# Kernel tuning notes

Measured on AMD Instinct MI355X. Metric: run time of the kernel, lower is better.

Reference implementation:

```python
import jax, jax.numpy as jnp
import numpy as np
import math

B, S, E, H = 4, 1024, 1024, 16
HD = E // H
MAX_SEQ = 5000
THETA = 10000.0


def _freqs_cis():
    # RotaryPositionalEncoding buffer: complex64 [MAX_SEQ, E//2]
    freqs = 1.0 / (THETA ** (np.arange(0, E, 2)[: E // 2] / E))
    ang = np.outer(np.arange(MAX_SEQ), freqs)
    return jnp.asarray(np.exp(1j * ang).astype(np.complex64))


def _rope(x, idx, fc_table):
    # x: [B, S, E]; pairs consecutive channels across the FULL embed_dim
    # (applied before head splitting, faithful to the original module)
    xc = x.reshape(*x.shape[:-1], -1, 2)
    xc = jax.lax.complex(xc[..., 0], xc[..., 1])  # [B, S, E//2]
    out = xc * fc_table[idx]                       # [B, S, E//2]
    return jnp.stack([jnp.real(out), jnp.imag(out)], axis=-1).reshape(x.shape)


def reference(query, key, value, query_index, key_index, attn_mask,
              key_padding_mask, Wq, bq, Wk, bk, Wv, bv, Wo, bo):
    q = query @ Wq.T + bq
    k = key @ Wk.T + bk
    v = value @ Wv.T + bv

    fc = _freqs_cis()
    q = _rope(q, query_index, fc)
    k = _rope(k, key_index, fc)

    # torch: q = cat(q.chunk(H, dim=-1), dim=0) -> flat HEAD-MAJOR [H*B, S, HD]
    qf = q.reshape(B, S, H, HD).transpose(2, 0, 1, 3).reshape(H * B, S, HD)
    kf = k.reshape(B, S, H, HD).transpose(2, 0, 1, 3).reshape(H * B, S, HD)
    vf = v.reshape(B, S, H, HD).transpose(2, 0, 1, 3).reshape(H * B, S, HD)

    # mask: logical_or(attn_mask[Sq,Sk], kpm[B,1,Sk]) -> [B, Sq, Sk]
    m = jnp.logical_or(attn_mask[None, :, :], key_padding_mask[:, None, :])
    madd = jnp.where(m, -jnp.inf, 0.0).astype(query.dtype)
    # torch repeat_interleave(H, dim=0) yields BATCH-MAJOR flat [B*H, Sq, Sk];
    # it is added to the head-major scores as-is (faithful to the original
    # indexing, including its head/batch-order quirk)
    madd_flat = jnp.repeat(madd, H, axis=0)

    scores = jnp.einsum('nqd,nkd->nqk', qf / math.sqrt(HD), kf) + madd_flat
    w = jax.nn.softmax(scores, axis=-1)              # [H*B, Sq, Sk]
    of = jnp.einsum('nqk,nkd->nqd', w, vf)           # [H*B, Sq, HD]

    # cat(chunks(dim=0), dim=-1) -> [B, Sq, E], head-major last dim
    attn_output = of.reshape(H, B, S, HD).transpose(1, 2, 0, 3).reshape(B, S, E)
    attn_output = attn_output @ Wo.T + bo

    # stack(chunks(dim=0), dim=1).mean(1) -> [B, Sq, Sk]
    attn_weights = w.reshape(H, B, S, S).transpose(1, 0, 2, 3).mean(axis=1)
    return attn_output, attn_weights


def setup_inputs() -> dict:
    key0 = jax.random.key(0)
    ks = jax.random.split(key0, 10)
    sc = 0.02
    inp = {
        'query': jax.random.normal(ks[0], (B, S, E), jnp.float32),
        'key': jax.random.normal(ks[1], (B, S, E), jnp.float32),
        'value': jax.random.normal(ks[2], (B, S, E), jnp.float32),
        'query_index': jnp.sort(jax.random.randint(ks[3], (B, S), 0, 4096), axis=-1),
        'key_index': jnp.sort(jax.random.randint(ks[4], (B, S), 0, 4096), axis=-1),
        'attn_mask': jnp.triu(jnp.ones((S, S), jnp.bool_), k=1),  # causal
        'key_padding_mask': jnp.zeros((B, S), jnp.bool_),
        'Wq': jax.random.normal(ks[5], (E, E), jnp.float32) * sc,
        'bq': jnp.zeros((E,), jnp.float32),
        'Wk': jax.random.normal(ks[6], (E, E), jnp.float32) * sc,
        'bk': jnp.zeros((E,), jnp.float32),
        'Wv': jax.random.normal(ks[7], (E, E), jnp.float32) * sc,
        'bv': jnp.zeros((E,), jnp.float32),
        'Wo': jax.random.normal(ks[8], (E, E), jnp.float32) * sc,
        'bo': jnp.zeros((E,), jnp.float32),
    }
    return inp
```

## Files before the change

kernel.cpp:

```cpp
#include <hip/hip_runtime.h>
#include <stdint.h>
#include <math.h>

#define B_ 4
#define S_ 1024
#define E_ 1024
#define H_ 16
#define HD_ 64
#define HB_ 64

typedef __attribute__((ext_vector_type(8))) short bhalf8;
typedef __attribute__((ext_vector_type(4))) float floatx4;

__device__ __forceinline__ unsigned short f2bf(float f) {
  union { float f; unsigned u; } v; v.f = f;
  unsigned r = (v.u + 0x7FFFu + ((v.u >> 16) & 1u)) >> 16;
  return (unsigned short)r;
}
__device__ __forceinline__ float bf2f(unsigned short b) {
  union { unsigned u; float f; } v; v.u = ((unsigned)b) << 16;
  return v.f;
}
__device__ __forceinline__ unsigned cvtpk_bf16(float a, float b) {
  unsigned r;
  asm volatile("v_cvt_pk_bf16_f32 %0, %1, %2" : "=v"(r) : "v"(a), "v"(b));
  return r;
}

__device__ __forceinline__ void gload16(const void* g, void* l) {
  __builtin_amdgcn_global_load_lds(
      (const __attribute__((address_space(1))) unsigned int*)g,
      (__attribute__((address_space(3))) unsigned int*)l, 16, 0, 0);
}

template <int NCH>
__device__ __forceinline__ void stage_tile(const unsigned short* org,
                                           unsigned short* lds, int wave, int lane) {
  const int rl = lane >> 3;
  const int scb = ((lane & 7) << 4) ^ (rl << 4);
  const char* base = (const char*)org + scb;
#pragma unroll
  for (int i = 0; i < NCH / 4; ++i) {
    const int c = wave + 4 * i;
    gload16(base + (size_t)(c * 8 + rl) * 2048, (char*)lds + c * 1024);
  }
}

__device__ __forceinline__ bhalf8 read_frag(const unsigned short* lds, int row, int kbyte) {
  const int off = row * 128 + (kbyte ^ ((row & 7) << 4));
  return *(const bhalf8*)((const char*)lds + off);
}

__global__ void detect_bool_kernel(const uint8_t* __restrict__ amask, int* __restrict__ flag) {
  if (threadIdx.x == 0 && blockIdx.x == 0) *flag = (amask[1] != 0) ? 1 : 0;
}

__global__ __launch_bounds__(256) void mprep_kernel(
    const void* __restrict__ amask, const void* __restrict__ kpm,
    const int* __restrict__ flagp, unsigned long long* __restrict__ Mbits) {
  const int gid = blockIdx.x * 256 + threadIdx.x;
  const int word = gid & 15, q = (gid >> 4) & 1023, bp = gid >> 14;
  const int k0 = word * 64;
  unsigned long long bits = 0;
  if (*flagp) {
    const uint8_t* ap = (const uint8_t*)amask + (size_t)q * 1024 + k0;
    const uint8_t* kp = (const uint8_t*)kpm + (size_t)bp * 1024 + k0;
#pragma unroll
    for (int c = 0; c < 4; ++c) {
      uint4 a = *(const uint4*)(ap + c * 16);
      uint4 k = *(const uint4*)(kp + c * 16);
      unsigned aw[4] = {a.x | k.x, a.y | k.y, a.z | k.z, a.w | k.w};
#pragma unroll
      for (int wv = 0; wv < 4; ++wv)
#pragma unroll
        for (int bt = 0; bt < 4; ++bt)
          if ((aw[wv] >> (8 * bt)) & 0xffu)
            bits |= 1ull << (c * 16 + wv * 4 + bt);
    }
  } else {
    const int* ap = (const int*)amask + (size_t)q * 1024 + k0;
    const int* kp = (const int*)kpm + (size_t)bp * 1024 + k0;
#pragma unroll
    for (int c = 0; c < 16; ++c) {
      int4 a = *(const int4*)(ap + c * 4);
      int4 k = *(const int4*)(kp + c * 4);
      if (a.x | k.x) bits |= 1ull << (c * 4 + 0);
      if (a.y | k.y) bits |= 1ull << (c * 4 + 1);
      if (a.z | k.z) bits |= 1ull << (c * 4 + 2);
      if (a.w | k.w) bits |= 1ull << (c * 4 + 3);
    }
  }
  Mbits[((size_t)bp << 14) + (size_t)q * 16 + word] = bits;
}

__global__ __launch_bounds__(256) void cvt_in_kernel(
    const float* __restrict__ q, const float* __restrict__ k,
    const float* __restrict__ v, unsigned short* __restrict__ Ab) {
  const int z = blockIdx.z;
  const float* src = (z == 0) ? q : (z == 1) ? k : v;
  unsigned short* dst = Ab + (size_t)z * 4194304;
  const size_t i = ((size_t)blockIdx.x * 256 + threadIdx.x) * 8;
  float4 a = *(const float4*)(src + i);
  float4 b = *(const float4*)(src + i + 4);
  bhalf8 r;
  r[0] = (short)f2bf(a.x); r[1] = (short)f2bf(a.y);
  r[2] = (short)f2bf(a.z); r[3] = (short)f2bf(a.w);
  r[4] = (short)f2bf(b.x); r[5] = (short)f2bf(b.y);
  r[6] = (short)f2bf(b.z); r[7] = (short)f2bf(b.w);
  *(bhalf8*)(dst + i) = r;
}

__global__ __launch_bounds__(256) void cvt_w_kernel(
    const float* __restrict__ wq, const float* __restrict__ wk,
    const float* __restrict__ wv, const float* __restrict__ wo,
    unsigned short* __restrict__ Wb) {
  const int z = blockIdx.z;
  const float* src = (z == 0) ? wq : (z == 1) ? wk : (z == 2) ? wv : wo;
  unsigned short* dst = Wb + (size_t)z * 1048576;
  const size_t i = ((size_t)blockIdx.x * 256 + threadIdx.x) * 8;
  float4 a = *(const float4*)(src + i);
  float4 b = *(const float4*)(src + i + 4);
  bhalf8 r;
  r[0] = (short)f2bf(a.x); r[1] = (short)f2bf(a.y);
  r[2] = (short)f2bf(a.z); r[3] = (short)f2bf(a.w);
  r[4] = (short)f2bf(b.x); r[5] = (short)f2bf(b.y);
  r[6] = (short)f2bf(b.z); r[7] = (short)f2bf(b.w);
  *(bhalf8*)(dst + i) = r;
}

template <bool BF16OUT>
__global__ __launch_bounds__(256) void mfma_gemm_kernel(
    const unsigned short* __restrict__ A0, const unsigned short* __restrict__ A1,
    const unsigned short* __restrict__ A2,
    const unsigned short* __restrict__ W0, const unsigned short* __restrict__ W1,
    const unsigned short* __restrict__ W2,
    const float* __restrict__ b0, const float* __restrict__ b1,
    const float* __restrict__ b2,
    void* __restrict__ C0, void* __restrict__ C1, void* __restrict__ C2) {
  const int z = blockIdx.z;
  const unsigned short* A = (z == 0) ? A0 : (z == 1) ? A1 : A2;
  const unsigned short* W = (z == 0) ? W0 : (z == 1) ? W1 : W2;
  const float* bias = (z == 0) ? b0 : (z == 1) ? b1 : b2;
  void* C = (z == 0) ? C0 : (z == 1) ? C1 : C2;
  const int lin = blockIdx.y * 8 + blockIdx.x;
  const int swz = (lin & 7) * 32 + (lin >> 3);
  const int m0 = (swz >> 3) * 128, n0 = (swz & 7) * 128;
  __shared__ unsigned short As[128 * 64];
  __shared__ unsigned short Ws[128 * 64];
  const int t = threadIdx.x, wave = t >> 6, lane = t & 63;
  const int wr = wave >> 1, wc = wave & 1;
  floatx4 acc[4][4];
  const floatx4 z4 = {0.f, 0.f, 0.f, 0.f};
#pragma unroll
  for (int i = 0; i < 4; ++i)
#pragma unroll
    for (int j = 0; j < 4; ++j) acc[i][j] = z4;

  for (int k0 = 0; k0 < 1024; k0 += 64) {
    stage_tile<16>(A + (size_t)m0 * 1024 + k0, As, wave, lane);
    stage_tile<16>(W + (size_t)n0 * 1024 + k0, Ws, wave, lane);
    __syncthreads();
#pragma unroll
    for (int ks = 0; ks < 2; ++ks) {
      const int kb = ks * 64 + ((lane >> 4) << 4);
      bhalf8 af[4], bf[4];
#pragma unroll
      for (int mi = 0; mi < 4; ++mi)
        af[mi] = read_frag(As, wr * 64 + mi * 16 + (lane & 15), kb);
#pragma unroll
      for (int ni = 0; ni < 4; ++ni)
        bf[ni] = read_frag(Ws, wc * 64 + ni * 16 + (lane & 15), kb);
#pragma unroll
      for (int mi = 0; mi < 4; ++mi)
#pragma unroll
        for (int ni = 0; ni < 4; ++ni)
          acc[mi][ni] = __builtin_amdgcn_mfma_f32_16x16x32_bf16(af[mi], bf[ni], acc[mi][ni], 0, 0, 0);
    }
    __syncthreads();
  }
#pragma unroll
  for (int mi = 0; mi < 4; ++mi)
#pragma unroll
    for (int ni = 0; ni < 4; ++ni) {
      const int col = n0 + wc * 64 + ni * 16 + (lane & 15);
      const float bv = bias[col];
#pragma unroll
      for (int r = 0; r < 4; ++r) {
        const int row = m0 + wr * 64 + mi * 16 + (lane >> 4) * 4 + r;
        const float v = acc[mi][ni][r] + bv;
        if (BF16OUT)
          ((unsigned short*)C)[(size_t)row * 1024 + col] = f2bf(v);
        else
          ((float*)C)[(size_t)row * 1024 + col] = v;
      }
    }
}

__global__ __launch_bounds__(256) void rope_bf_kernel(unsigned int* __restrict__ X,
                                                      const int* __restrict__ idxs) {
  const int gid = blockIdx.x * 256 + threadIdx.x;
  const int i = gid & 511, bs = gid >> 9;
  const int pos = idxs[bs];
  const double freq = exp(-(double)(2 * i) * (9.210340371976184 / 1024.0));
  const double ang = fmod((double)pos * freq, 6.283185307179586476925287);
  const float fa = (float)ang;
  float sn, c;
  sincosf(fa, &sn, &c);
  const unsigned v = X[gid];
  const float x = bf2f((unsigned short)(v & 0xffffu));
  const float y = bf2f((unsigned short)(v >> 16));
  const float rx = x * c - y * sn;
  const float ry = x * sn + y * c;
  X[gid] = (unsigned)f2bf(rx) | ((unsigned)f2bf(ry) << 16);
}

__global__ __launch_bounds__(256) void transpose_v_kernel(
    const unsigned short* __restrict__ Vr, unsigned short* __restrict__ Vt) {
  const int s0 = blockIdx.x * 64;
  const int bh = blockIdx.y;
  const int b = bh >> 4, h = bh & 15;
  __shared__ unsigned short L[64][72];
  const int t = threadIdx.x, r = t >> 2, cq = (t & 3) * 16;
  const unsigned short* src = Vr + ((size_t)(b * S_) + s0 + r) * E_ + h * HD_ + cq;
  *(bhalf8*)&L[r][cq] = *(const bhalf8*)src;
  *(bhalf8*)&L[r][cq + 8] = *(const bhalf8*)(src + 8);
  __syncthreads();
  bhalf8 o0, o1;
#pragma unroll
  for (int u = 0; u < 8; ++u) o0[u] = (short)L[cq + u][r];
#pragma unroll
  for (int u = 0; u < 8; ++u) o1[u] = (short)L[cq + 8 + u][r];
  unsigned short* dst = Vt + ((size_t)bh * 64 + r) * 1024 + s0 + cq;
  *(bhalf8*)dst = o0;
  *(bhalf8*)(dst + 8) = o1;
}

__global__ __launch_bounds__(256) void scores_sm_kernel(
    const unsigned short* __restrict__ Qr, const unsigned short* __restrict__ Kr,
    unsigned short* __restrict__ P, const unsigned long long* __restrict__ Mbits,
    int hb0, int nwg) {
  const int lin = blockIdx.y * 64 + blockIdx.x;
  const int q8 = nwg >> 3;
  const int swz = (lin & 7) * q8 + (lin >> 3);
  const int qb = swz & 63, lhb = swz >> 6;
  const int hb = hb0 + lhb;
  const int h = hb >> 2, b = hb & 3, bp = hb >> 4;
  const int q0 = qb * 16;
  __shared__ unsigned short Sbuf[16 * 1024];
  float* rptr = (float*)Sbuf;
  const int t = threadIdx.x, w = t >> 6, lane = t & 63;
  const int l4 = lane >> 4, l15 = lane & 15;

  const char* Qb = (const char*)Qr + ((size_t)b << 21) + h * 128;
  const char* Kb = (const char*)Kr + ((size_t)b << 21) + h * 128;

  const unsigned long long* mrow =
      Mbits + ((size_t)bp << 14) + (size_t)(q0 + l15) * 16 + w * 4;
  unsigned long long mw0 = mrow[0], mw1 = mrow[1], mw2 = mrow[2], mw3 = mrow[3];

  bhalf8 bq0 = *(const bhalf8*)(Qb + (size_t)(q0 + l15) * 2048 + l4 * 16);
  bhalf8 bq1 = *(const bhalf8*)(Qb + (size_t)(q0 + l15) * 2048 + 64 + l4 * 16);

  floatx4 acc[16];
  const floatx4 z4 = {0.f, 0.f, 0.f, 0.f};
#pragma unroll
  for (int i = 0; i < 16; ++i) acc[i] = z4;
#pragma unroll
  for (int mt = 0; mt < 16; ++mt) {
    const char* kr = Kb + (size_t)(w * 256 + mt * 16 + l15) * 2048 + l4 * 16;
    bhalf8 a0 = *(const bhalf8*)kr;
    bhalf8 a1 = *(const bhalf8*)(kr + 64);
    acc[mt] = __builtin_amdgcn_mfma_f32_16x16x32_bf16(a0, bq0, acc[mt], 0, 0, 0);
    acc[mt] = __builtin_amdgcn_mfma_f32_16x16x32_bf16(a1, bq1, acc[mt], 0, 0, 0);
  }

  float red[16];
#pragma unroll
  for (int mt = 0; mt < 16; ++mt)
    red[mt] = fmaxf(fmaxf(acc[mt][0], acc[mt][1]), fmaxf(acc[mt][2], acc[mt][3]));
#pragma unroll
  for (int s2 = 8; s2 > 0; s2 >>= 1)
#pragma unroll
    for (int i = 0; i < 8; ++i)
      if (i < s2) red[i] = fmaxf(red[i], red[i + s2]);
  float mx = red[0];
  mx = fmaxf(mx, __shfl_xor(mx, 16));
  mx = fmaxf(mx, __shfl_xor(mx, 32));
  if (l4 == 0) rptr[w * 16 + l15] = mx;
  __syncthreads();
  mx = fmaxf(fmaxf(rptr[l15], rptr[16 + l15]), fmaxf(rptr[32 + l15], rptr[48 + l15]));

  const float Cc = 0.18033688011112042f;
  const float mc = mx * Cc;
#pragma unroll
  for (int mt = 0; mt < 16; ++mt) {
    const unsigned long long mwv = (mt < 4) ? mw0 : (mt < 8) ? mw1 : (mt < 12) ? mw2 : mw3;
    const unsigned bits = (unsigned)(mwv >> ((mt & 3) * 16 + l4 * 4)) & 0xFu;
#pragma unroll
    for (int r = 0; r < 4; ++r) {
      float e = exp2f(__builtin_fmaf(acc[mt][r], Cc, -mc));
      acc[mt][r] = ((bits >> r) & 1u) ? 0.f : e;
    }
  }

#pragma unroll
  for (int mt = 0; mt < 16; ++mt)
    red[mt] = (acc[mt][0] + acc[mt][1]) + (acc[mt][2] + acc[mt][3]);
#pragma unroll
  for (int s2 = 8; s2 > 0; s2 >>= 1)
#pragma unroll
    for (int i = 0; i < 8; ++i)
      if (i < s2) red[i] += red[i + s2];
  float sm = red[0];
  sm += __shfl_xor(sm, 16);
  sm += __shfl_xor(sm, 32);
  if (l4 == 0) rptr[64 + w * 16 + l15] = sm;
  __syncthreads();
  sm = (rptr[64 + l15] + rptr[80 + l15]) + (rptr[96 + l15] + rptr[112 + l15]);
  const float inv = 1.0f / sm;
  __syncthreads();

  const int xr = (l15 & 7) << 4;
#pragma unroll
  for (int mt = 0; mt < 16; ++mt) {
    uint2 pk;
    pk.x = cvtpk_bf16(acc[mt][0] * inv, acc[mt][1] * inv);
    pk.y = cvtpk_bf16(acc[mt][2] * inv, acc[mt][3] * inv);
    const int kb2 = (w * 256 + mt * 16 + l4 * 4) * 2;
    *(uint2*)((char*)Sbuf + l15 * 2048 + (kb2 ^ xr)) = pk;
  }
  __syncthreads();

  unsigned short* pbase = P + ((size_t)lhb << 20);
#pragma unroll
  for (int rr = 0; rr < 4; ++rr) {
    const int ql = w * 4 + rr;
    const int gq = q0 + ql;
    const int xq = (ql & 7) << 4;
#pragma unroll
    for (int j = 0; j < 2; ++j) {
      bhalf8 v = *(const bhalf8*)((const char*)Sbuf + ql * 2048 +
                                  ((j * 1024 + lane * 16) ^ xq));
      *(bhalf8*)(pbase + ((size_t)gq << 10) + j * 512 + lane * 8) = v;
    }
  }
}

__global__ __launch_bounds__(256) void wmean_kernel(
    const unsigned short* __restrict__ P, float* __restrict__ outW,
    int nhh, int first) {
  const size_t gid = (size_t)blockIdx.x * 256 + threadIdx.x;
  const int k8 = (int)(gid & 127);
  const int q = (int)((gid >> 7) & 1023);
  const int b = (int)(gid >> 17);
  float s[8];
#pragma unroll
  for (int u = 0; u < 8; ++u) s[u] = 0.f;
  for (int hh = 0; hh < nhh; ++hh) {
    const int lhb = hh * 4 + b;
    bhalf8 v = *(const bhalf8*)(P + ((size_t)lhb << 20) + ((size_t)q << 10) + k8 * 8);
#pragma unroll
    for (int u = 0; u < 8; ++u) s[u] += bf2f((unsigned short)v[u]);
  }
  float* o = outW + (((size_t)(b * S_ + q)) << 10) + k8 * 8;
  const float invH = 1.0f / 16.0f;
  float4 v0, v1;
  v0.x = s[0] * invH; v0.y = s[1] * invH; v0.z = s[2] * invH; v0.w = s[3] * invH;
  v1.x = s[4] * invH; v1.y = s[5] * invH; v1.z = s[6] * invH; v1.w = s[7] * invH;
  if (!first) {
    float4 a = *(float4*)o, b4 = *(float4*)(o + 4);
    v0.x += a.x; v0.y += a.y; v0.z += a.z; v0.w += a.w;
    v1.x += b4.x; v1.y += b4.y; v1.z += b4.z; v1.w += b4.w;
  }
  *(float4*)o = v0;
  *(float4*)(o + 4) = v1;
}

__global__ __launch_bounds__(256) void pv_mfma_kernel(
    const unsigned short* __restrict__ Wt, const unsigned short* __restrict__ Vt,
    unsigned short* __restrict__ Ocat, int hb0, int nwg) {
  const int lin = blockIdx.y * 16 + blockIdx.x;
  const int q8 = nwg >> 3;
  const int swz = (lin & 7) * q8 + (lin >> 3);
  const int qt = swz & 15, lhb = swz >> 4;
  const int hb = hb0 + lhb;
  const int h = hb >> 2, b = hb & 3;
  const int q0 = qt * 64;
  __shared__ unsigned short Ps[64 * 64];
  __shared__ unsigned short Vs[64 * 64];
  const int t = threadIdx.x, wave = t >> 6, lane = t & 63;
  const int wr = wave >> 1, wc = wave & 1;
  const unsigned short* Wh = Wt + ((size_t)lhb << 20);
  const unsigned short* Vh = Vt + (size_t)(b * 16 + h) * 65536;
  floatx4 acc[2][2];
  const floatx4 z4 = {0.f, 0.f, 0.f, 0.f};
#pragma unroll
  for (int i = 0; i < 2; ++i)
#pragma unroll
    for (int j = 0; j < 2; ++j) acc[i][j] = z4;

  for (int k0 = 0; k0 < 1024; k0 += 64) {
    stage_tile<8>(Wh + (size_t)q0 * 1024 + k0, Ps, wave, lane);
    stage_tile<8>(Vh + k0, Vs, wave, lane);
    __syncthreads();
#pragma unroll
    for (int ks = 0; ks < 2; ++ks) {
      const int kb = ks * 64 + ((lane >> 4) << 4);
      bhalf8 af[2], bf[2];
#pragma unroll
      for (int mi = 0; mi < 2; ++mi)
        af[mi] = read_frag(Ps, wr * 32 + mi * 16 + (lane & 15), kb);
#pragma unroll
      for (int ni = 0; ni < 2; ++ni)
        bf[ni] = read_frag(Vs, wc * 32 + ni * 16 + (lane & 15), kb);
#pragma unroll
      for (int mi = 0; mi < 2; ++mi)
#pragma unroll
        for (int ni = 0; ni < 2; ++ni)
          acc[mi][ni] = __builtin_amdgcn_mfma_f32_16x16x32_bf16(af[mi], bf[ni], acc[mi][ni], 0, 0, 0);
    }
    __syncthreads();
  }
#pragma unroll
  for (int mi = 0; mi < 2; ++mi)
#pragma unroll
    for (int ni = 0; ni < 2; ++ni) {
      const int d = wc * 32 + ni * 16 + (lane & 15);
#pragma unroll
      for (int r = 0; r < 4; ++r) {
        const int q = q0 + wr * 32 + mi * 16 + (lane >> 4) * 4 + r;
        Ocat[((size_t)(b * S_) + q) * E_ + h * HD_ + d] = f2bf(acc[mi][ni][r]);
      }
    }
}

extern "C" void kernel_launch(void* const* d_in, const int* in_sizes, int n_in,
                              void* d_out, int out_size, void* d_ws, size_t ws_size,
                              hipStream_t stream) {
  (void)in_sizes; (void)n_in; (void)out_size;
  const float* query = (const float*)d_in[0];
  const float* key   = (const float*)d_in[1];
  const float* value = (const float*)d_in[2];
  const int* qidx = (const int*)d_in[3];
  const int* kidx = (const int*)d_in[4];
  const void* amask = d_in[5];
  const void* kpm   = d_in[6];
  const float* Wq = (const float*)d_in[7];
  const float* bq = (const float*)d_in[8];
  const float* Wk = (const float*)d_in[9];
  const float* bk = (const float*)d_in[10];
  const float* Wv = (const float*)d_in[11];
  const float* bv = (const float*)d_in[12];
  const float* Wo = (const float*)d_in[13];
  const float* bo = (const float*)d_in[14];

  float* outA = (float*)d_out;
  float* outW = (float*)d_out + (size_t)B_ * S_ * E_;

  float* ws = (float*)d_ws;
  unsigned short* Ab   = (unsigned short*)(ws + 0);
  unsigned short* Wb   = (unsigned short*)(ws + 6291456);
  unsigned short* Qr   = (unsigned short*)(ws + 8388608);
  unsigned short* Kr   = (unsigned short*)(ws + 10485760);
  unsigned short* Vr   = (unsigned short*)(ws + 12582912);
  unsigned short* Vt   = (unsigned short*)(ws + 14680064);
  unsigned short* Ocat = (unsigned short*)(ws + 16777216);
  int* flagp           = (int*)(ws + 18874368);
  unsigned long long* Mbits = (unsigned long long*)(ws + 18874432);
  const size_t tail_off = 18874432 + 131072;

  const size_t ws_floats = ws_size / 4;
  int CH = 0;
  unsigned short* P = nullptr;
  for (int c = 64; c >= 8; c >>= 1) {
    if (tail_off + (size_t)c * 524288 <= ws_floats) {
      CH = c;
      P = (unsigned short*)(ws + tail_off);
      break;
    }
  }
  if (!CH) {
    CH = 8;
    P = (unsigned short*)ws;
  }

  detect_bool_kernel<<<1, 64, 0, stream>>>((const uint8_t*)amask, flagp);
  mprep_kernel<<<256, 256, 0, stream>>>(amask, kpm, flagp, Mbits);

  cvt_in_kernel<<<dim3(2048, 1, 3), 256, 0, stream>>>(query, key, value, Ab);
  cvt_w_kernel<<<dim3(512, 1, 4), 256, 0, stream>>>(Wq, Wk, Wv, Wo, Wb);

  mfma_gemm_kernel<true><<<dim3(8, 32, 3), 256, 0, stream>>>(
      Ab, Ab + 4194304, Ab + 8388608,
      Wb, Wb + 1048576, Wb + 2097152,
      bq, bk, bv, Qr, Kr, Vr);

  rope_bf_kernel<<<8192, 256, 0, stream>>>((unsigned int*)Qr, qidx);
  rope_bf_kernel<<<8192, 256, 0, stream>>>((unsigned int*)Kr, kidx);

  transpose_v_kernel<<<dim3(16, 64), 256, 0, stream>>>(Vr, Vt);

  const int nch = HB_ / CH;
  for (int c = 0; c < nch; ++c) {
    const int hb0 = c * CH;
    scores_sm_kernel<<<dim3(64, CH), 256, 0, stream>>>(Qr, Kr, P, Mbits, hb0,
                                                       64 * CH);
    wmean_kernel<<<2048, 256, 0, stream>>>(P, outW, CH / 4, (c == 0) ? 1 : 0);
    pv_mfma_kernel<<<dim3(16, CH), 256, 0, stream>>>(P, Vt, Ocat, hb0, 16 * CH);
  }

  mfma_gemm_kernel<false><<<dim3(8, 32, 1), 256, 0, stream>>>(
      Ocat, Ocat, Ocat, Wb + 3145728, Wb + 3145728, Wb + 3145728,
      bo, bo, bo, outA, outA, outA);
}
```

Measured before the change: 241.3 us.

## Fuse conversion launches, write V transposed from GEMM, merge RoPE in float

Merges the input and weight bf16 conversion kernels into one launch and the two RoPE launches into one. The QKV GEMM epilogue now stores V directly in the per-head transposed layout, removing the separate transpose kernel. The GEMM block swizzle is extended across the z dimension, and the RoPE angle is computed in single precision with exp2f instead of double exp/fmod. This cuts launches, memory passes and FP64 work, at the cost of lower angle precision for large positions and strided stores in the V epilogue.

```diff
diff --git a/kernel.cpp b/kernel.cpp
--- a/kernel.cpp
+++ b/kernel.cpp
@@ -93,12 +93,24 @@
   Mbits[((size_t)bp << 14) + (size_t)q * 16 + word] = bits;
 }
 
-__global__ __launch_bounds__(256) void cvt_in_kernel(
+__global__ __launch_bounds__(256) void cvt_all_kernel(
     const float* __restrict__ q, const float* __restrict__ k,
-    const float* __restrict__ v, unsigned short* __restrict__ Ab) {
+    const float* __restrict__ v,
+    const float* __restrict__ wq, const float* __restrict__ wk,
+    const float* __restrict__ wv, const float* __restrict__ wo,
+    unsigned short* __restrict__ Ab, unsigned short* __restrict__ Wb) {
   const int z = blockIdx.z;
-  const float* src = (z == 0) ? q : (z == 1) ? k : v;
-  unsigned short* dst = Ab + (size_t)z * 4194304;
+  if (z >= 3 && blockIdx.x >= 512) return;
+  const float* src;
+  unsigned short* dst;
+  if (z < 3) {
+    src = (z == 0) ? q : (z == 1) ? k : v;
+    dst = Ab + (size_t)z * 4194304;
+  } else {
+    const int zz = z - 3;
+    src = (zz == 0) ? wq : (zz == 1) ? wk : (zz == 2) ? wv : wo;
+    dst = Wb + (size_t)zz * 1048576;
+  }
   const size_t i = ((size_t)blockIdx.x * 256 + threadIdx.x) * 8;
   float4 a = *(const float4*)(src + i);
   float4 b = *(const float4*)(src + i + 4);
@@ -110,25 +122,7 @@
   *(bhalf8*)(dst + i) = r;
 }
 
-__global__ __launch_bounds__(256) void cvt_w_kernel(
-    const float* __restrict__ wq, const float* __restrict__ wk,
-    const float* __restrict__ wv, const float* __restrict__ wo,
-    unsigned short* __restrict__ Wb) {
-  const int z = blockIdx.z;
-  const float* src = (z == 0) ? wq : (z == 1) ? wk : (z == 2) ? wv : wo;
-  unsigned short* dst = Wb + (size_t)z * 1048576;
-  const size_t i = ((size_t)blockIdx.x * 256 + threadIdx.x) * 8;
-  float4 a = *(const float4*)(src + i);
-  float4 b = *(const float4*)(src + i + 4);
-  bhalf8 r;
-  r[0] = (short)f2bf(a.x); r[1] = (short)f2bf(a.y);
-  r[2] = (short)f2bf(a.z); r[3] = (short)f2bf(a.w);
-  r[4] = (short)f2bf(b.x); r[5] = (short)f2bf(b.y);
-  r[6] = (short)f2bf(b.z); r[7] = (short)f2bf(b.w);
-  *(bhalf8*)(dst + i) = r;
-}
-
-template <bool BF16OUT>
+template <bool QKV>
 __global__ __launch_bounds__(256) void mfma_gemm_kernel(
     const unsigned short* __restrict__ A0, const unsigned short* __restrict__ A1,
     const unsigned short* __restrict__ A2,
@@ -137,18 +131,22 @@
     const float* __restrict__ b0, const float* __restrict__ b1,
     const float* __restrict__ b2,
     void* __restrict__ C0, void* __restrict__ C1, void* __restrict__ C2) {
-  const int z = blockIdx.z;
-  const unsigned short* A = (z == 0) ? A0 : (z == 1) ? A1 : A2;
-  const unsigned short* W = (z == 0) ? W0 : (z == 1) ? W1 : W2;
-  const float* bias = (z == 0) ? b0 : (z == 1) ? b1 : b2;
-  void* C = (z == 0) ? C0 : (z == 1) ? C1 : C2;
-  const int lin = blockIdx.y * 8 + blockIdx.x;
-  const int swz = (lin & 7) * 32 + (lin >> 3);
-  const int m0 = (swz >> 3) * 128, n0 = (swz & 7) * 128;
+  const int nb = gridDim.z * 256;
+  const int chunk = nb >> 3;
+  const int g = blockIdx.z * 256 + blockIdx.y * 8 + blockIdx.x;
+  const int swz = (g & 7) * chunk + (g >> 3);
+  const int zt = swz >> 8;
+  const int r8 = swz & 255;
+  const int m0 = (r8 >> 3) * 128, n0 = (r8 & 7) * 128;
+  const unsigned short* A = (zt == 0) ? A0 : (zt == 1) ? A1 : A2;
+  const unsigned short* W = (zt == 0) ? W0 : (zt == 1) ? W1 : W2;
+  const float* bias = (zt == 0) ? b0 : (zt == 1) ? b1 : b2;
+  void* C = (zt == 0) ? C0 : (zt == 1) ? C1 : C2;
   __shared__ unsigned short As[128 * 64];
   __shared__ unsigned short Ws[128 * 64];
   const int t = threadIdx.x, wave = t >> 6, lane = t & 63;
   const int wr = wave >> 1, wc = wave & 1;
+  const int l4 = lane >> 4, l15 = lane & 15;
   floatx4 acc[4][4];
   const floatx4 z4 = {0.f, 0.f, 0.f, 0.f};
 #pragma unroll
@@ -162,14 +160,14 @@
     __syncthreads();
 #pragma unroll
     for (int ks = 0; ks < 2; ++ks) {
-      const int kb = ks * 64 + ((lane >> 4) << 4);
+      const int kb = ks * 64 + (l4 << 4);
       bhalf8 af[4], bf[4];
 #pragma unroll
       for (int mi = 0; mi < 4; ++mi)
-        af[mi] = read_frag(As, wr * 64 + mi * 16 + (lane & 15), kb);
+        af[mi] = read_frag(As, wr * 64 + mi * 16 + l15, kb);
 #pragma unroll
       for (int ni = 0; ni < 4; ++ni)
-        bf[ni] = read_frag(Ws, wc * 64 + ni * 16 + (lane & 15), kb);
+        bf[ni] = read_frag(Ws, wc * 64 + ni * 16 + l15, kb);
 #pragma unroll
       for (int mi = 0; mi < 4; ++mi)
 #pragma unroll
@@ -178,61 +176,65 @@
     }
     __syncthreads();
   }
-#pragma unroll
-  for (int mi = 0; mi < 4; ++mi)
-#pragma unroll
-    for (int ni = 0; ni < 4; ++ni) {
-      const int col = n0 + wc * 64 + ni * 16 + (lane & 15);
-      const float bv = bias[col];
-#pragma unroll
-      for (int r = 0; r < 4; ++r) {
-        const int row = m0 + wr * 64 + mi * 16 + (lane >> 4) * 4 + r;
-        const float v = acc[mi][ni][r] + bv;
-        if (BF16OUT)
-          ((unsigned short*)C)[(size_t)row * 1024 + col] = f2bf(v);
-        else
-          ((float*)C)[(size_t)row * 1024 + col] = v;
+
+  if (QKV && zt == 2) {
+#pragma unroll
+    for (int mi = 0; mi < 4; ++mi) {
+      const int row0 = m0 + wr * 64 + mi * 16 + l4 * 4;
+      const int b = row0 >> 10, s = row0 & 1023;
+#pragma unroll
+      for (int ni = 0; ni < 4; ++ni) {
+        const int col = n0 + wc * 64 + ni * 16 + l15;
+        const int h = col >> 6, d = col & 63;
+        const float bv = bias[col];
+        ushort4 o;
+        o.x = f2bf(acc[mi][ni][0] + bv);
+        o.y = f2bf(acc[mi][ni][1] + bv);
+        o.z = f2bf(acc[mi][ni][2] + bv);
+        o.w = f2bf(acc[mi][ni][3] + bv);
+        *(ushort4*)((unsigned short*)C +
+                    (((size_t)(b * 16 + h) * 64 + d) << 10) + s) = o;
       }
     }
-}
-
-__global__ __launch_bounds__(256) void rope_bf_kernel(unsigned int* __restrict__ X,
-                                                      const int* __restrict__ idxs) {
+  } else {
+#pragma unroll
+    for (int mi = 0; mi < 4; ++mi)
+#pragma unroll
+      for (int ni = 0; ni < 4; ++ni) {
+        const int col = n0 + wc * 64 + ni * 16 + l15;
+        const float bv = bias[col];
+#pragma unroll
+        for (int r = 0; r < 4; ++r) {
+          const int row = m0 + wr * 64 + mi * 16 + l4 * 4 + r;
+          const float v = acc[mi][ni][r] + bv;
+          if (QKV)
+            ((unsigned short*)C)[(size_t)row * 1024 + col] = f2bf(v);
+          else
+            ((float*)C)[(size_t)row * 1024 + col] = v;
+        }
+      }
+  }
+}
+
+__global__ __launch_bounds__(256) void rope_bf_kernel(
+    unsigned int* __restrict__ Q, unsigned int* __restrict__ K,
+    const int* __restrict__ qidx, const int* __restrict__ kidx) {
+  const int z = blockIdx.y;
+  unsigned int* X = z ? K : Q;
+  const int* idxs = z ? kidx : qidx;
   const int gid = blockIdx.x * 256 + threadIdx.x;
   const int i = gid & 511, bs = gid >> 9;
   const int pos = idxs[bs];
-  const double freq = exp(-(double)(2 * i) * (9.210340371976184 / 1024.0));
-  const double ang = fmod((double)pos * freq, 6.283185307179586476925287);
-  const float fa = (float)ang;
+  const float fr = exp2f((float)i * (-13.287712379549449f / 512.0f));
+  const float ang = (float)pos * fr;
   float sn, c;
-  sincosf(fa, &sn, &c);
+  sincosf(ang, &sn, &c);
   const unsigned v = X[gid];
   const float x = bf2f((unsigned short)(v & 0xffffu));
   const float y = bf2f((unsigned short)(v >> 16));
   const float rx = x * c - y * sn;
   const float ry = x * sn + y * c;
   X[gid] = (unsigned)f2bf(rx) | ((unsigned)f2bf(ry) << 16);
-}
-
-__global__ __launch_bounds__(256) void transpose_v_kernel(
-    const unsigned short* __restrict__ Vr, unsigned short* __restrict__ Vt) {
-  const int s0 = blockIdx.x * 64;
-  const int bh = blockIdx.y;
-  const int b = bh >> 4, h = bh & 15;
-  __shared__ unsigned short L[64][72];
-  const int t = threadIdx.x, r = t >> 2, cq = (t & 3) * 16;
-  const unsigned short* src = Vr + ((size_t)(b * S_) + s0 + r) * E_ + h * HD_ + cq;
-  *(bhalf8*)&L[r][cq] = *(const bhalf8*)src;
-  *(bhalf8*)&L[r][cq + 8] = *(const bhalf8*)(src + 8);
-  __syncthreads();
-  bhalf8 o0, o1;
-#pragma unroll
-  for (int u = 0; u < 8; ++u) o0[u] = (short)L[cq + u][r];
-#pragma unroll
-  for (int u = 0; u < 8; ++u) o1[u] = (short)L[cq + 8 + u][r];
-  unsigned short* dst = Vt + ((size_t)bh * 64 + r) * 1024 + s0 + cq;
-  *(bhalf8*)dst = o0;
-  *(bhalf8*)(dst + 8) = o1;
 }
 
 __global__ __launch_bounds__(256) void scores_sm_kernel(
@@ -462,7 +464,6 @@
   unsigned short* Wb   = (unsigned short*)(ws + 6291456);
   unsigned short* Qr   = (unsigned short*)(ws + 8388608);
   unsigned short* Kr   = (unsigned short*)(ws + 10485760);
-  unsigned short* Vr   = (unsigned short*)(ws + 12582912);
   unsigned short* Vt   = (unsigned short*)(ws + 14680064);
   unsigned short* Ocat = (unsigned short*)(ws + 16777216);
   int* flagp           = (int*)(ws + 18874368);
@@ -487,18 +488,16 @@
   detect_bool_kernel<<<1, 64, 0, stream>>>((const uint8_t*)amask, flagp);
   mprep_kernel<<<256, 256, 0, stream>>>(amask, kpm, flagp, Mbits);
 
-  cvt_in_kernel<<<dim3(2048, 1, 3), 256, 0, stream>>>(query, key, value, Ab);
-  cvt_w_kernel<<<dim3(512, 1, 4), 256, 0, stream>>>(Wq, Wk, Wv, Wo, Wb);
+  cvt_all_kernel<<<dim3(2048, 1, 7), 256, 0, stream>>>(
+      query, key, value, Wq, Wk, Wv, Wo, Ab, Wb);
 
   mfma_gemm_kernel<true><<<dim3(8, 32, 3), 256, 0, stream>>>(
       Ab, Ab + 4194304, Ab + 8388608,
       Wb, Wb + 1048576, Wb + 2097152,
-      bq, bk, bv, Qr, Kr, Vr);
-
-  rope_bf_kernel<<<8192, 256, 0, stream>>>((unsigned int*)Qr, qidx);
-  rope_bf_kernel<<<8192, 256, 0, stream>>>((unsigned int*)Kr, kidx);
-
-  transpose_v_kernel<<<dim3(16, 64), 256, 0, stream>>>(Vr, Vt);
+      bq, bk, bv, Qr, Kr, Vt);
+
+  rope_bf_kernel<<<dim3(8192, 2), 256, 0, stream>>>(
+      (unsigned int*)Qr, (unsigned int*)Kr, qidx, kidx);
 
   const int nch = HB_ / CH;
   for (int c = 0; c < nch; ++c) {
```

New measurement: 252.7 us. 1.05x slower.
